# Performance work log

Hardware: AMD Instinct MI355X
Metric: run time of the kernel (lower is better)

Reference implementation:

```python
import jax, jax.numpy as jnp
import numpy as np

B, S = 8, 512          # batch, seq_len
D, F = 1024, 2048      # d_model, head hidden dim
H = 16                 # num_tasks (= num heads)
V = 3000               # selfies vocab
O = 1                  # head output size
INIT = 0.02


def setup_inputs() -> dict:
    key = jax.random.key(0)
    ks = jax.random.split(key, 12)
    return {
        "selfies": jax.random.randint(ks[0], (B, S), 0, V),
        "tasks": jax.random.randint(ks[1], (B, S), 0, H + 1),  # 0 -> invalid (-1)
        "values": jax.random.normal(ks[2], (B, S), jnp.float32),
        "property_mask": jax.random.randint(ks[3], (B, S), 0, 2).astype(bool),
        # shared_base params (embed + FFN -> [B,S,D])
        "emb_selfies": jax.random.normal(ks[4], (V, D), jnp.float32) * INIT,
        "emb_tasks": jax.random.normal(ks[5], (H + 1, D), jnp.float32) * INIT,
        "val_vec": jax.random.normal(ks[6], (D,), jnp.float32) * INIT,
        "Ws": jax.random.normal(ks[7], (D, D), jnp.float32) * INIT,
        "bs": jnp.zeros((D,), jnp.float32),
        # stacked per-head MLP params: Linear(D,F) -> GELU -> Linear(F,O)
        "W1": jax.random.normal(ks[8], (H, D, F), jnp.float32) * INIT,
        "b1": jnp.zeros((H, F), jnp.float32),
        "W2": jax.random.normal(ks[9], (H, F, O), jnp.float32) * INIT,
        "b2": jnp.zeros((H, O), jnp.float32),
    }


def reference(selfies, tasks, values, property_mask,
              emb_selfies, emb_tasks, val_vec, Ws, bs, W1, b1, W2, b2):
    # ---- shared_base: embed + masked token features + FFN -> [B,S,D] ----
    h = (emb_selfies[selfies] + emb_tasks[tasks] + values[..., None] * val_vec)
    h = h * property_mask[..., None].astype(h.dtype)
    shared = jax.nn.gelu(h @ Ws + bs)                      # [B,S,D]

    # ---- routing: task token -> head index, 0 means invalid (-1) ----
    head_idx = jnp.where(tasks > 0, (tasks - 1) % H, -1)   # [B,S]

    # ---- each active head runs its MLP over the FULL shared_output ----
    hid = jax.nn.gelu(jnp.einsum('bsd,hdf->bshf', shared, W1) + b1)  # [B,S,H,F]
    heads_out = jnp.einsum('bshf,hfo->bsho', hid, W2) + b2           # [B,S,H,O]

    # ---- scatter/select per token by head index; invalid -> zeros ----
    idx = jnp.clip(head_idx, 0)
    out = jnp.take_along_axis(heads_out, idx[..., None, None], axis=2)[:, :, 0, :]
    return jnp.where(head_idx[..., None] >= 0, out, jnp.zeros_like(out))
```

## Files before the change

### kernel.cpp

```cpp
#include <hip/hip_runtime.h>
#include <hip/hip_bf16.h>

#define TOK 4096
#define DD  1024
#define FF  2048
#define NH  16

typedef short bf16x8 __attribute__((ext_vector_type(8)));
typedef float f32x4  __attribute__((ext_vector_type(4)));

__device__ __forceinline__ float gelu_f(float x) {
  float u = 0.7978845608028654f * (x + 0.044715f * x * x * x);
  float e = __expf(2.0f * u);
  return 0.5f * x * (2.0f - 2.0f / (e + 1.0f));
}

__device__ __forceinline__ unsigned short f2bf(float f) {
  union { float f; unsigned u; } v; v.f = f;
  unsigned r = v.u + 0x7FFF + ((v.u >> 16) & 1);
  return (unsigned short)(r >> 16);
}
__device__ __forceinline__ unsigned pack2(float a, float b) {
  return (unsigned)f2bf(a) | ((unsigned)f2bf(b) << 16);
}

__device__ __forceinline__ void load_lds16(const void* g, void* l) {
  __builtin_amdgcn_global_load_lds(
      (const __attribute__((address_space(1))) void*)g,
      (__attribute__((address_space(3))) void*)l, 16, 0, 0);
}

#define W1_TILES (16 * 16 * 32)
#define WS_TILES (16 * 16)
#define PW_BLKS  (W1_TILES + WS_TILES)
#define PX_BLKS  (TOK * 128 / 256)

__device__ void prep_w_body(
    int bid, const float* __restrict__ Ws, const float* __restrict__ W1,
    unsigned short* __restrict__ Wsp, unsigned short* __restrict__ W1p) {
  __shared__ unsigned short T[64][70];
  const float* src; unsigned short* dstBase; int stride, nt0, kc0;
  if (bid < W1_TILES) {
    int fb = bid & 31, kb = (bid >> 5) & 15, h = bid >> 9;
    src = W1 + ((size_t)h * DD + kb * 64) * FF + fb * 64;
    stride = FF;
    nt0 = h * 128 + fb * 4;
    kc0 = kb * 2;
    dstBase = W1p;
  } else {
    int b2 = bid - W1_TILES;
    int fb = b2 & 15, kb = b2 >> 4;
    src = Ws + (size_t)(kb * 64) * DD + fb * 64;
    stride = DD;
    nt0 = fb * 4;
    kc0 = kb * 2;
    dstBase = Wsp;
  }
  const int tid = threadIdx.x;
  {
    int r = tid >> 2, cq = (tid & 3) * 16;
    const float* p = src + (size_t)r * stride + cq;
#pragma unroll
    for (int i = 0; i < 4; ++i) {
      float4 v = *(const float4*)(p + i * 4);
      *(unsigned*)&T[r][cq + i * 4 + 0] = pack2(v.x, v.y);
      *(unsigned*)&T[r][cq + i * 4 + 2] = pack2(v.z, v.w);
    }
  }
  __syncthreads();
#pragma unroll
  for (int cc = 0; cc < 2; ++cc) {
    int idx = tid + cc * 256;
    int lane2 = idx & 63, kcl = (idx >> 6) & 1, ntl = idx >> 7;
    int n_local = ntl * 16 + (lane2 & 15);
    int r0 = kcl * 32 + (lane2 >> 4) * 8;
    unsigned short e[8];
#pragma unroll
    for (int j = 0; j < 8; ++j) e[j] = T[r0 + j][n_local];
    uint4 o;
    o.x = (unsigned)e[0] | ((unsigned)e[1] << 16);
    o.y = (unsigned)e[2] | ((unsigned)e[3] << 16);
    o.z = (unsigned)e[4] | ((unsigned)e[5] << 16);
    o.w = (unsigned)e[6] | ((unsigned)e[7] << 16);
    size_t chunk = ((size_t)(nt0 + ntl) * 32 + (kc0 + kcl)) * 64 + lane2;
    *(uint4*)(dstBase + chunk * 8) = o;
  }
}

__device__ void prep_x_body(
    int gid, const int* __restrict__ selfies, const int* __restrict__ tasks,
    const float* __restrict__ values, const int* __restrict__ pmask,
    const float* __restrict__ emb_s, const float* __restrict__ emb_t,
    const float* __restrict__ val_vec, unsigned short* __restrict__ Xb) {
  int kc = (gid & 127) * 8;
  int t  = gid >> 7;
  int sid = selfies[t], tsk = tasks[t];
  float v = values[t];
  float msk = pmask[t] ? 1.0f : 0.0f;
  const float* ps = emb_s + (size_t)sid * DD + kc;
  const float* pt = emb_t + (size_t)tsk * DD + kc;
  const float* pv = val_vec + kc;
  float r[8];
#pragma unroll
  for (int j = 0; j < 8; j += 4) {
    float4 a = *(const float4*)(ps + j);
    float4 b = *(const float4*)(pt + j);
    float4 c = *(const float4*)(pv + j);
    r[j + 0] = (a.x + b.x + v * c.x) * msk;
    r[j + 1] = (a.y + b.y + v * c.y) * msk;
    r[j + 2] = (a.z + b.z + v * c.z) * msk;
    r[j + 3] = (a.w + b.w + v * c.w) * msk;
  }
  uint4 o;
  o.x = pack2(r[0], r[1]); o.y = pack2(r[2], r[3]);
  o.z = pack2(r[4], r[5]); o.w = pack2(r[6], r[7]);
  *(uint4*)(Xb + (size_t)gid * 8) = o;
}

__global__ __launch_bounds__(256) void prep_all(
    const int* __restrict__ selfies, const int* __restrict__ tasks,
    const float* __restrict__ values, const int* __restrict__ pmask,
    const float* __restrict__ emb_s, const float* __restrict__ emb_t,
    const float* __restrict__ val_vec, const float* __restrict__ Ws,
    const float* __restrict__ W1, const float* __restrict__ b2,
    unsigned short* __restrict__ Xb, unsigned short* __restrict__ Wsp,
    unsigned short* __restrict__ W1p,
    int* __restrict__ counts, int* __restrict__ lists, float* __restrict__ out) {
  int bid = blockIdx.x;
  if (bid < PW_BLKS) {
    prep_w_body(bid, Ws, W1, Wsp, W1p);
  } else if (bid < PW_BLKS + PX_BLKS) {
    prep_x_body((bid - PW_BLKS) * 256 + threadIdx.x,
                selfies, tasks, values, pmask, emb_s, emb_t, val_vec, Xb);
  } else {
    int t = (bid - PW_BLKS - PX_BLKS) * 256 + threadIdx.x;
    if (t < TOK) {
      int task = tasks[t];
      if (task > 0) {
        int h = (task - 1) & (NH - 1);
        int pos = atomicAdd(&counts[h], 1);
        lists[h * TOK + pos] = t;
        out[t] = b2[h];
      } else {
        out[t] = 0.0f;
      }
    }
  }
}

__global__ __launch_bounds__(256) void gemm1_mfma(
    const unsigned short* __restrict__ Xb, const unsigned short* __restrict__ Wsp,
    const float* __restrict__ bs, unsigned short* __restrict__ shared_bf) {
  __shared__ __align__(16) unsigned short As[4][4 * 64 * 8];
  __shared__ __align__(16) unsigned short Bs[4][8 * 64 * 8];

  const int tid = threadIdx.x;
  const int lane = tid & 63, w = tid >> 6;
  const int m0 = blockIdx.x * 64;
  const int n0 = blockIdx.y * 128;
  const int q = lane >> 4, c = lane & 15;

  const unsigned short* aSrc = Xb + (size_t)(m0 + w * 16 + c) * DD + q * 8;
  const unsigned short* bBase = Wsp + ((size_t)(blockIdx.y * 8 + w * 2)) * 32 * 512 + lane * 8;
  f32x4 acc[4][2] = {};

  float bsv[2];
  bsv[0] = bs[n0 + w * 32 + c];
  bsv[1] = bs[n0 + w * 32 + 16 + c];
  asm volatile("" :: "v"(bsv[0]), "v"(bsv[1]));

  auto stage = [&](int buf, int kc2) {
    load_lds16(aSrc + kc2 * 32, As[buf] + (size_t)(w * 64 + lane) * 8);
    const unsigned short* bk = bBase + kc2 * 512;
    load_lds16(bk,            Bs[buf] + (size_t)((w * 2 + 0) * 64 + lane) * 8);
    load_lds16(bk + 16384,    Bs[buf] + (size_t)((w * 2 + 1) * 64 + lane) * 8);
  };
  auto compute = [&](int buf) {
    bf16x8 a[4], b[2];
#pragma unroll
    for (int mt = 0; mt < 4; ++mt)
      a[mt] = *(const bf16x8*)(As[buf] + (size_t)(mt * 64 + lane) * 8);
#pragma unroll
    for (int t = 0; t < 2; ++t)
      b[t] = *(const bf16x8*)(Bs[buf] + (size_t)((w * 2 + t) * 64 + lane) * 8);
    __builtin_amdgcn_s_setprio(1);
#pragma unroll
    for (int mt = 0; mt < 4; ++mt)
#pragma unroll
      for (int t = 0; t < 2; ++t)
        acc[mt][t] = __builtin_amdgcn_mfma_f32_16x16x32_bf16(a[mt], b[t], acc[mt][t], 0, 0, 0);
    __builtin_amdgcn_s_setprio(0);
  };

  stage(0, 0);
  stage(1, 1);
  for (int i = 0; i < 30; ++i) {
    stage((i + 2) & 3, i + 2);
    asm volatile("s_waitcnt vmcnt(6)" ::: "memory");
    __builtin_amdgcn_s_barrier();
    compute(i & 3);
    asm volatile("" ::: "memory");
  }
  asm volatile("s_waitcnt vmcnt(3)" ::: "memory");
  __builtin_amdgcn_s_barrier();
  compute(2);
  asm volatile("" ::: "memory");
  asm volatile("s_waitcnt vmcnt(0)" ::: "memory");
  __builtin_amdgcn_s_barrier();
  compute(3);

#pragma unroll
  for (int mt = 0; mt < 4; ++mt)
#pragma unroll
    for (int t = 0; t < 2; ++t)
#pragma unroll
      for (int r = 0; r < 4; ++r) {
        int row = m0 + mt * 16 + q * 4 + r;
        int col = n0 + w * 32 + t * 16 + c;
        shared_bf[(size_t)row * DD + col] = f2bf(gelu_f(acc[mt][t][r] + bsv[t]));
      }
}

__global__ __launch_bounds__(256) void gemm2_mfma(
    const unsigned short* __restrict__ shared_bf, const unsigned short* __restrict__ W1p,
    const float* __restrict__ b1, const float* __restrict__ W2,
    const int* __restrict__ counts, const int* __restrict__ lists,
    float* __restrict__ out) {
  const int id = blockIdx.x;
  const int xcd = id & 7, local_ = id >> 3;
  const int h = xcd + 8 * (local_ >> 7);
  const int rest = local_ & 127;
  const int fc = rest & 15;
  const int m0 = (rest >> 4) * 64;
  const int nt_h = counts[h];
  if (m0 >= nt_h) return;

  __shared__ __align__(16) unsigned short As[4][4 * 64 * 8];
  __shared__ __align__(16) unsigned short Bs[4][8 * 64 * 8];
  __shared__ int   stok[64];
  __shared__ float red[4][68];

  const int tid = threadIdx.x;
  const int lane = tid & 63, w = tid >> 6;
  const int q = lane >> 4, c = lane & 15;

  if (tid < 64) {
    int i = m0 + tid;
    stok[tid] = (i < nt_h) ? lists[h * TOK + i] : -1;
  }
  __syncthreads();

  int tokr = stok[w * 16 + c];
  if (tokr < 0) tokr = 0;
  const unsigned short* aSrc = shared_bf + (size_t)tokr * DD + q * 8;
  const unsigned short* bBase =
      W1p + ((size_t)h * 128 + fc * 8 + w * 2) * 32 * 512 + lane * 8;

  f32x4 acc[4][2] = {};

  const float* b1h = b1 + (size_t)h * FF + fc * 128 + w * 32;
  const float* w2h = W2 + (size_t)h * FF + fc * 128 + w * 32;
  float b1v[2], w2v[2];
  b1v[0] = b1h[c];      b1v[1] = b1h[16 + c];
  w2v[0] = w2h[c];      w2v[1] = w2h[16 + c];
  asm volatile("" :: "v"(b1v[0]), "v"(b1v[1]), "v"(w2v[0]), "v"(w2v[1]));

  auto stage = [&](int buf, int kc2) {
    load_lds16(aSrc + kc2 * 32, As[buf] + (size_t)(w * 64 + lane) * 8);
    const unsigned short* bk = bBase + kc2 * 512;
    load_lds16(bk,            Bs[buf] + (size_t)((w * 2 + 0) * 64 + lane) * 8);
    load_lds16(bk + 16384,    Bs[buf] + (size_t)((w * 2 + 1) * 64 + lane) * 8);
  };
  auto compute = [&](int buf) {
    bf16x8 a[4], b[2];
#pragma unroll
    for (int mt = 0; mt < 4; ++mt)
      a[mt] = *(const bf16x8*)(As[buf] + (size_t)(mt * 64 + lane) * 8);
#pragma unroll
    for (int t = 0; t < 2; ++t)
      b[t] = *(const bf16x8*)(Bs[buf] + (size_t)((w * 2 + t) * 64 + lane) * 8);
    __builtin_amdgcn_s_setprio(1);
#pragma unroll
    for (int mt = 0; mt < 4; ++mt)
#pragma unroll
      for (int t = 0; t < 2; ++t)
        acc[mt][t] = __builtin_amdgcn_mfma_f32_16x16x32_bf16(a[mt], b[t], acc[mt][t], 0, 0, 0);
    __builtin_amdgcn_s_setprio(0);
  };

  stage(0, 0);
  stage(1, 1);
  for (int i = 0; i < 30; ++i) {
    stage((i + 2) & 3, i + 2);
    asm volatile("s_waitcnt vmcnt(6)" ::: "memory");
    __builtin_amdgcn_s_barrier();
    compute(i & 3);
    asm volatile("" ::: "memory");
  }
  asm volatile("s_waitcnt vmcnt(3)" ::: "memory");
  __builtin_amdgcn_s_barrier();
  compute(2);
  asm volatile("" ::: "memory");
  asm volatile("s_waitcnt vmcnt(0)" ::: "memory");
  __builtin_amdgcn_s_barrier();
  compute(3);

#pragma unroll
  for (int mt = 0; mt < 4; ++mt)
#pragma unroll
    for (int r = 0; r < 4; ++r) {
      float s = 0.0f;
#pragma unroll
      for (int t = 0; t < 2; ++t)
        s += gelu_f(acc[mt][t][r] + b1v[t]) * w2v[t];
      s += __shfl_xor(s, 1);
      s += __shfl_xor(s, 2);
      s += __shfl_xor(s, 4);
      s += __shfl_xor(s, 8);
      if (c == 0) red[w][mt * 16 + q * 4 + r] = s;
    }
  __syncthreads();

  if (tid < 64) {
    int t = stok[tid];
    if (t >= 0) {
      float s = red[0][tid] + red[1][tid] + red[2][tid] + red[3][tid];
      atomicAdd(&out[t], s);
    }
  }
}

extern "C" void kernel_launch(void* const* d_in, const int* in_sizes, int n_in,
                              void* d_out, int out_size, void* d_ws, size_t ws_size,
                              hipStream_t stream) {
  const int*   selfies = (const int*)d_in[0];
  const int*   tasks   = (const int*)d_in[1];
  const float* values  = (const float*)d_in[2];
  const int*   pmask   = (const int*)d_in[3];
  const float* emb_s   = (const float*)d_in[4];
  const float* emb_t   = (const float*)d_in[5];
  const float* val_vec = (const float*)d_in[6];
  const float* Ws      = (const float*)d_in[7];
  const float* bs      = (const float*)d_in[8];
  const float* W1      = (const float*)d_in[9];
  const float* b1      = (const float*)d_in[10];
  const float* W2      = (const float*)d_in[11];
  const float* b2      = (const float*)d_in[12];
  float* out = (float*)d_out;

  char* ws = (char*)d_ws;
  unsigned short* Xb        = (unsigned short*)ws;
  unsigned short* shared_bf = (unsigned short*)(ws + (8u << 20));
  unsigned short* Wsp       = (unsigned short*)(ws + (16u << 20));
  unsigned short* W1p       = (unsigned short*)(ws + (18u << 20));
  int* counts = (int*)(ws + (82u << 20));
  int* lists  = (int*)(ws + (82u << 20) + 256);

  hipMemsetAsync(counts, 0, NH * sizeof(int), stream);
  prep_all<<<PW_BLKS + PX_BLKS + TOK / 256, 256, 0, stream>>>(
      selfies, tasks, values, pmask, emb_s, emb_t, val_vec, Ws, W1, b2,
      Xb, Wsp, W1p, counts, lists, out);
  gemm1_mfma<<<dim3(TOK / 64, DD / 128), 256, 0, stream>>>(Xb, Wsp, bs, shared_bf);
  gemm2_mfma<<<2048, 256, 0, stream>>>(shared_bf, W1p, b1, W2,
                                       counts, lists, out);
}
```

Measured before the change: 304.2 us.

## Overlap W1 bf16 conversion with gemm1 by co-scheduling in one kernel

W1 fp32-to-bf16 repacking moves out of the prep kernel into the same launch as the first GEMM, so the 8192 conversion blocks run alongside the 512 GEMM blocks instead of delaying the GEMM. The prep kernel keeps only the small Ws conversion, embedding build and routing, so the first GEMM can start sooner. In exchange, the merged kernel reserves a fixed 48KB shared buffer for every block, which may lower occupancy for the conversion blocks. GEMM blocks may also compete with them for memory bandwidth.

New measurement: 304.4 us. No clear change (+0.1%).

```diff
diff --git a/kernel.cpp b/kernel.cpp
--- a/kernel.cpp
+++ b/kernel.cpp
@@ -30,32 +30,10 @@
       (__attribute__((address_space(3))) void*)l, 16, 0, 0);
 }
 
-#define W1_TILES (16 * 16 * 32)
-#define WS_TILES (16 * 16)
-#define PW_BLKS  (W1_TILES + WS_TILES)
-#define PX_BLKS  (TOK * 128 / 256)
-
-__device__ void prep_w_body(
-    int bid, const float* __restrict__ Ws, const float* __restrict__ W1,
-    unsigned short* __restrict__ Wsp, unsigned short* __restrict__ W1p) {
-  __shared__ unsigned short T[64][70];
-  const float* src; unsigned short* dstBase; int stride, nt0, kc0;
-  if (bid < W1_TILES) {
-    int fb = bid & 31, kb = (bid >> 5) & 15, h = bid >> 9;
-    src = W1 + ((size_t)h * DD + kb * 64) * FF + fb * 64;
-    stride = FF;
-    nt0 = h * 128 + fb * 4;
-    kc0 = kb * 2;
-    dstBase = W1p;
-  } else {
-    int b2 = bid - W1_TILES;
-    int fb = b2 & 15, kb = b2 >> 4;
-    src = Ws + (size_t)(kb * 64) * DD + fb * 64;
-    stride = DD;
-    nt0 = fb * 4;
-    kc0 = kb * 2;
-    dstBase = Wsp;
-  }
+__device__ __forceinline__ void wtile_convert(
+    const float* __restrict__ src, int stride,
+    unsigned short* __restrict__ dstBase, int nt0, int kc0,
+    unsigned short (*T)[70]) {
   const int tid = threadIdx.x;
   {
     int r = tid >> 2, cq = (tid & 3) * 16;
@@ -87,53 +65,50 @@
   }
 }
 
-__device__ void prep_x_body(
-    int gid, const int* __restrict__ selfies, const int* __restrict__ tasks,
-    const float* __restrict__ values, const int* __restrict__ pmask,
-    const float* __restrict__ emb_s, const float* __restrict__ emb_t,
-    const float* __restrict__ val_vec, unsigned short* __restrict__ Xb) {
-  int kc = (gid & 127) * 8;
-  int t  = gid >> 7;
-  int sid = selfies[t], tsk = tasks[t];
-  float v = values[t];
-  float msk = pmask[t] ? 1.0f : 0.0f;
-  const float* ps = emb_s + (size_t)sid * DD + kc;
-  const float* pt = emb_t + (size_t)tsk * DD + kc;
-  const float* pv = val_vec + kc;
-  float r[8];
-#pragma unroll
-  for (int j = 0; j < 8; j += 4) {
-    float4 a = *(const float4*)(ps + j);
-    float4 b = *(const float4*)(pt + j);
-    float4 c = *(const float4*)(pv + j);
-    r[j + 0] = (a.x + b.x + v * c.x) * msk;
-    r[j + 1] = (a.y + b.y + v * c.y) * msk;
-    r[j + 2] = (a.z + b.z + v * c.z) * msk;
-    r[j + 3] = (a.w + b.w + v * c.w) * msk;
-  }
-  uint4 o;
-  o.x = pack2(r[0], r[1]); o.y = pack2(r[2], r[3]);
-  o.z = pack2(r[4], r[5]); o.w = pack2(r[6], r[7]);
-  *(uint4*)(Xb + (size_t)gid * 8) = o;
-}
-
-__global__ __launch_bounds__(256) void prep_all(
+#define WS_BLKS 256
+#define PX_BLKS (TOK * 128 / 256)
+
+__global__ __launch_bounds__(256) void prep_small(
     const int* __restrict__ selfies, const int* __restrict__ tasks,
     const float* __restrict__ values, const int* __restrict__ pmask,
     const float* __restrict__ emb_s, const float* __restrict__ emb_t,
     const float* __restrict__ val_vec, const float* __restrict__ Ws,
-    const float* __restrict__ W1, const float* __restrict__ b2,
+    const float* __restrict__ b2,
     unsigned short* __restrict__ Xb, unsigned short* __restrict__ Wsp,
-    unsigned short* __restrict__ W1p,
     int* __restrict__ counts, int* __restrict__ lists, float* __restrict__ out) {
+  __shared__ unsigned short T[64][70];
   int bid = blockIdx.x;
-  if (bid < PW_BLKS) {
-    prep_w_body(bid, Ws, W1, Wsp, W1p);
-  } else if (bid < PW_BLKS + PX_BLKS) {
-    prep_x_body((bid - PW_BLKS) * 256 + threadIdx.x,
-                selfies, tasks, values, pmask, emb_s, emb_t, val_vec, Xb);
+  if (bid < WS_BLKS) {
+    int fb = bid & 15, kb = bid >> 4;
+    wtile_convert(Ws + (size_t)(kb * 64) * DD + fb * 64, DD, Wsp,
+                  fb * 4, kb * 2, T);
+  } else if (bid < WS_BLKS + PX_BLKS) {
+    int gid = (bid - WS_BLKS) * 256 + threadIdx.x;
+    int kc = (gid & 127) * 8;
+    int t  = gid >> 7;
+    int sid = selfies[t], tsk = tasks[t];
+    float v = values[t];
+    float msk = pmask[t] ? 1.0f : 0.0f;
+    const float* ps = emb_s + (size_t)sid * DD + kc;
+    const float* pt = emb_t + (size_t)tsk * DD + kc;
+    const float* pv = val_vec + kc;
+    float r[8];
+#pragma unroll
+    for (int j = 0; j < 8; j += 4) {
+      float4 a = *(const float4*)(ps + j);
+      float4 b = *(const float4*)(pt + j);
+      float4 c = *(const float4*)(pv + j);
+      r[j + 0] = (a.x + b.x + v * c.x) * msk;
+      r[j + 1] = (a.y + b.y + v * c.y) * msk;
+      r[j + 2] = (a.z + b.z + v * c.z) * msk;
+      r[j + 3] = (a.w + b.w + v * c.w) * msk;
+    }
+    uint4 o;
+    o.x = pack2(r[0], r[1]); o.y = pack2(r[2], r[3]);
+    o.z = pack2(r[4], r[5]); o.w = pack2(r[6], r[7]);
+    *(uint4*)(Xb + (size_t)gid * 8) = o;
   } else {
-    int t = (bid - PW_BLKS - PX_BLKS) * 256 + threadIdx.x;
+    int t = (bid - WS_BLKS - PX_BLKS) * 256 + threadIdx.x;
     if (t < TOK) {
       int task = tasks[t];
       if (task > 0) {
@@ -148,20 +123,25 @@
   }
 }
 
-__global__ __launch_bounds__(256) void gemm1_mfma(
-    const unsigned short* __restrict__ Xb, const unsigned short* __restrict__ Wsp,
-    const float* __restrict__ bs, unsigned short* __restrict__ shared_bf) {
-  __shared__ __align__(16) unsigned short As[4][4 * 64 * 8];
-  __shared__ __align__(16) unsigned short Bs[4][8 * 64 * 8];
+#define G1_BLKS  512
+#define W1_BLKS  (16 * 16 * 32)
+
+__device__ void gemm1_body(
+    int bid, const unsigned short* __restrict__ Xb,
+    const unsigned short* __restrict__ Wsp, const float* __restrict__ bs,
+    unsigned short* __restrict__ shared_bf, char* smem) {
+  unsigned short* As = (unsigned short*)smem;
+  unsigned short* Bs = (unsigned short*)(smem + 16384);
 
   const int tid = threadIdx.x;
   const int lane = tid & 63, w = tid >> 6;
-  const int m0 = blockIdx.x * 64;
-  const int n0 = blockIdx.y * 128;
+  const int m0 = (bid & 63) * 64;
+  const int n0 = (bid >> 6) * 128;
   const int q = lane >> 4, c = lane & 15;
 
   const unsigned short* aSrc = Xb + (size_t)(m0 + w * 16 + c) * DD + q * 8;
-  const unsigned short* bBase = Wsp + ((size_t)(blockIdx.y * 8 + w * 2)) * 32 * 512 + lane * 8;
+  const unsigned short* bBase =
+      Wsp + ((size_t)((bid >> 6) * 8 + w * 2)) * 32 * 512 + lane * 8;
   f32x4 acc[4][2] = {};
 
   float bsv[2];
@@ -170,19 +150,19 @@
   asm volatile("" :: "v"(bsv[0]), "v"(bsv[1]));
 
   auto stage = [&](int buf, int kc2) {
-    load_lds16(aSrc + kc2 * 32, As[buf] + (size_t)(w * 64 + lane) * 8);
+    load_lds16(aSrc + kc2 * 32, As + buf * 2048 + (size_t)(w * 64 + lane) * 8);
     const unsigned short* bk = bBase + kc2 * 512;
-    load_lds16(bk,            Bs[buf] + (size_t)((w * 2 + 0) * 64 + lane) * 8);
-    load_lds16(bk + 16384,    Bs[buf] + (size_t)((w * 2 + 1) * 64 + lane) * 8);
+    load_lds16(bk,         Bs + buf * 4096 + (size_t)((w * 2 + 0) * 64 + lane) * 8);
+    load_lds16(bk + 16384, Bs + buf * 4096 + (size_t)((w * 2 + 1) * 64 + lane) * 8);
   };
   auto compute = [&](int buf) {
     bf16x8 a[4], b[2];
 #pragma unroll
     for (int mt = 0; mt < 4; ++mt)
-      a[mt] = *(const bf16x8*)(As[buf] + (size_t)(mt * 64 + lane) * 8);
+      a[mt] = *(const bf16x8*)(As + buf * 2048 + (size_t)(mt * 64 + lane) * 8);
 #pragma unroll
     for (int t = 0; t < 2; ++t)
-      b[t] = *(const bf16x8*)(Bs[buf] + (size_t)((w * 2 + t) * 64 + lane) * 8);
+      b[t] = *(const bf16x8*)(Bs + buf * 4096 + (size_t)((w * 2 + t) * 64 + lane) * 8);
     __builtin_amdgcn_s_setprio(1);
 #pragma unroll
     for (int mt = 0; mt < 4; ++mt)
@@ -219,6 +199,23 @@
         int col = n0 + w * 32 + t * 16 + c;
         shared_bf[(size_t)row * DD + col] = f2bf(gelu_f(acc[mt][t][r] + bsv[t]));
       }
+}
+
+__global__ __launch_bounds__(256) void gemm1_w1prep(
+    const unsigned short* __restrict__ Xb, const unsigned short* __restrict__ Wsp,
+    const float* __restrict__ bs, unsigned short* __restrict__ shared_bf,
+    const float* __restrict__ W1, unsigned short* __restrict__ W1p) {
+  __shared__ __align__(16) char smem[49152];
+  int bid = blockIdx.x;
+  if (bid < G1_BLKS) {
+    gemm1_body(bid, Xb, Wsp, bs, shared_bf, smem);
+  } else {
+    int b = bid - G1_BLKS;
+    int fb = b & 31, kb = (b >> 5) & 15, h = b >> 9;
+    wtile_convert(W1 + ((size_t)h * DD + kb * 64) * FF + fb * 64, FF, W1p,
+                  h * 128 + fb * 4, kb * 2,
+                  (unsigned short (*)[70])smem);
+  }
 }
 
 __global__ __launch_bounds__(256) void gemm2_mfma(
@@ -357,10 +354,11 @@
   int* lists  = (int*)(ws + (82u << 20) + 256);
 
   hipMemsetAsync(counts, 0, NH * sizeof(int), stream);
-  prep_all<<<PW_BLKS + PX_BLKS + TOK / 256, 256, 0, stream>>>(
-      selfies, tasks, values, pmask, emb_s, emb_t, val_vec, Ws, W1, b2,
-      Xb, Wsp, W1p, counts, lists, out);
-  gemm1_mfma<<<dim3(TOK / 64, DD / 128), 256, 0, stream>>>(Xb, Wsp, bs, shared_bf);
+  prep_small<<<WS_BLKS + PX_BLKS + TOK / 256, 256, 0, stream>>>(
+      selfies, tasks, values, pmask, emb_s, emb_t, val_vec, Ws, b2,
+      Xb, Wsp, counts, lists, out);
+  gemm1_w1prep<<<G1_BLKS + W1_BLKS, 256, 0, stream>>>(
+      Xb, Wsp, bs, shared_bf, W1, W1p);
   gemm2_mfma<<<2048, 256, 0, stream>>>(shared_bf, W1p, b1, W2,
                                        counts, lists, out);
 }
```
